# Optimization experiments

Measured on AMD Instinct MI355X. Metric: run time of the kernel, lower is better.

The kernel has to match this reference:

```python
import jax, jax.numpy as jnp
import numpy as np

N_GOOD = 16
NUM_TEST = 16
NUM_UNITS = 32
EPS = 1e-5


def _mlp(x, w1, b1, w2, b2):
    # Linear -> ReLU -> Linear -> ReLU
    h = jax.nn.relu(x @ w1 + b1)
    return jax.nn.relu(h @ w2 + b2)


def _ln_relu(x, g, b):
    mu = jnp.mean(x, axis=-1, keepdims=True)
    var = jnp.mean(jnp.square(x - mu), axis=-1, keepdims=True)
    return jax.nn.relu((x - mu) / jnp.sqrt(var + EPS) * g + b)


def _attend(self_out, enc):
    # self_out: [B, D], enc: [B, N, D]
    scores = jnp.einsum('bd,bnd->bn', self_out, enc) / np.float32(np.sqrt(NUM_TEST))
    attn = jax.nn.softmax(scores, axis=-1)
    return jnp.einsum('bn,bnd->bd', attn, enc)


def setup_inputs() -> dict:
    key = jax.random.key(0)
    ks = jax.random.split(key, 24)
    B = 262144
    obs_dim = 4 + (N_GOOD - 1) * 5 + N_GOOD * 3  # 127

    def lin(k, fan_in, fan_out):
        bound = 1.0 / np.sqrt(fan_in)
        kw, kb = jax.random.split(k)
        w = jax.random.uniform(kw, (fan_in, fan_out), jnp.float32, -bound, bound)
        b = jax.random.uniform(kb, (fan_out,), jnp.float32, -bound, bound)
        return w, b

    en_w1, en_b1 = lin(ks[0], 4, NUM_UNITS)
    en_w2, en_b2 = lin(ks[1], NUM_UNITS, NUM_TEST)
    oa_w1, oa_b1 = lin(ks[2], 5, NUM_UNITS)
    oa_w2, oa_b2 = lin(ks[3], NUM_UNITS, NUM_TEST)
    g_w1, g_b1 = lin(ks[4], 3, NUM_UNITS)
    g_w2, g_b2 = lin(ks[5], NUM_UNITS, NUM_TEST)
    m_w1, m_b1 = lin(ks[6], NUM_TEST * 3, NUM_UNITS)
    m_w2, m_b2 = lin(ks[7], NUM_UNITS, NUM_UNITS)
    m_w3, m_b3 = lin(ks[8], NUM_UNITS, 2)

    return {
        's_input': jax.random.normal(ks[9], (B, obs_dim), jnp.float32),
        'en_w1': en_w1, 'en_b1': en_b1, 'en_w2': en_w2, 'en_b2': en_b2,
        'oa_w1': oa_w1, 'oa_b1': oa_b1, 'oa_w2': oa_w2, 'oa_b2': oa_b2,
        'oa_g': jnp.ones((NUM_TEST,), jnp.float32), 'oa_bln': jnp.zeros((NUM_TEST,), jnp.float32),
        'g_w1': g_w1, 'g_b1': g_b1, 'g_w2': g_w2, 'g_b2': g_b2,
        'g_g': jnp.ones((NUM_TEST,), jnp.float32), 'g_bln': jnp.zeros((NUM_TEST,), jnp.float32),
        'm_w1': m_w1, 'm_b1': m_b1, 'm_w2': m_w2, 'm_b2': m_b2, 'm_w3': m_w3, 'm_b3': m_b3,
    }


def reference(s_input, en_w1, en_b1, en_w2, en_b2,
              oa_w1, oa_b1, oa_w2, oa_b2, oa_g, oa_bln,
              g_w1, g_b1, g_w2, g_b2, g_g, g_bln,
              m_w1, m_b1, m_w2, m_b2, m_w3, m_b3):
    n = N_GOOD
    B = s_input.shape[0]

    # self encoding: [B, 16]
    self_out = _mlp(s_input[:, :4], en_w1, en_b1, en_w2, en_b2)

    # other agents: width (n-1)*5 = [pos pairs | vel pairs | scalar per agent]
    og = s_input[:, 4:4 + (n - 1) * 5]
    pos = og[:, :(n - 1) * 2].reshape(B, n - 1, 2)
    vel = og[:, (n - 1) * 2:(n - 1) * 4].reshape(B, n - 1, 2)
    scal = og[:, (n - 1) * 4:(n - 1) * 5].reshape(B, n - 1, 1)
    other_in = jnp.concatenate([pos, vel, scal], axis=-1)  # [B, n-1, 5]
    other_enc = _mlp(other_in, oa_w1, oa_b1, oa_w2, oa_b2)  # [B, n-1, 16]
    other_out = _ln_relu(_attend(self_out, other_enc), oa_g, oa_bln)

    # food/goals: last n*3 cols, chunks of 3
    food_in = s_input[:, -n * 3:].reshape(B, n, 3)
    food_enc = _mlp(food_in, g_w1, g_b1, g_w2, g_b2)  # [B, n, 16]
    food_out = _ln_relu(_attend(self_out, food_enc), g_g, g_bln)

    merged = jnp.concatenate([self_out, food_out, other_out], axis=1)  # [B, 48]
    h = jax.nn.leaky_relu(merged @ m_w1 + m_b1, 0.01)
    h = jax.nn.leaky_relu(h @ m_w2 + m_b2, 0.01)
    return jnp.tanh(h @ m_w3 + m_b3)  # [B, 2]
```

## Files before the change

### kernel.cpp

```cpp
#include <hip/hip_runtime.h>
#include <math.h>


#define OBS 127
#define XSS 132

typedef _Float16 v4h  __attribute__((ext_vector_type(4)));
typedef __fp16   p2h  __attribute__((ext_vector_type(2)));
typedef float    v16f __attribute__((ext_vector_type(16)));
typedef float    f4u  __attribute__((ext_vector_type(4), aligned(4)));

#define MFMA32(a, b, c) __builtin_amdgcn_mfma_f32_32x32x8f16((a), (b), (c), 0, 0, 0)

union PK { p2h p[2]; v4h h; uint2 u; };
union HU { unsigned u[2]; v4h h; };

__device__ __forceinline__ v4h zero4h() {
    v4h z; z[0] = z[1] = z[2] = z[3] = (_Float16)0.f; return z;
}
__device__ __forceinline__ v4h pack4(float a, float b, float c, float d) {
    PK q;
    q.p[0] = __builtin_amdgcn_cvt_pkrtz(a, b);
    q.p[1] = __builtin_amdgcn_cvt_pkrtz(c, d);
    return q.h;
}
__device__ __forceinline__ v4h a1frag(const float* __restrict__ W,
                                      const float* __restrict__ b,
                                      int kin, int m, int h) {
    v4h r;
    #pragma unroll
    for (int j = 0; j < 4; ++j) {
        const int k = 4 * h + j;
        const float v = (k < kin) ? W[k * 32 + m] : (k == kin ? b[m] : 0.f);
        r[j] = (_Float16)v;
    }
    return r;
}
__device__ __forceinline__ v4h a2frag(const float* __restrict__ W2,
                                      int s, int m, int h) {
    v4h r;
    #pragma unroll
    for (int j = 0; j < 4; ++j) {
        const int k = 8 * s + 4 * h + j;
        r[j] = (_Float16)((m < 16) ? W2[k * 16 + m] : 0.f);
    }
    return r;
}
__device__ __forceinline__ v4h wfrag(const float* __restrict__ W, int ncols,
                                     int K, int s, int m, int h, int colmax) {
    v4h r;
    #pragma unroll
    for (int j = 0; j < 4; ++j) {
        const int k = 8 * s + 4 * h + j;
        r[j] = (_Float16)((k < K && m < colmax) ? W[k * ncols + m] : 0.f);
    }
    return r;
}
__device__ __forceinline__ v4h bfragA(const float* __restrict__ b, int m, int h, int colmax) {
    v4h r = zero4h();
    if (h == 0 && m < colmax) r[0] = (_Float16)b[m];
    return r;
}
__device__ __forceinline__ float fast_tanh(float x) {
    x = fminf(fmaxf(x, -15.f), 15.f);
    const float ex = __expf(2.f * x);
    return (ex - 1.f) / (ex + 1.f);
}

template <int BR>
__device__ __forceinline__ void entity_step(const _Float16* __restrict__ xr,
                                            int e, int h,
                                            v4h A1, const v4h (&A2)[4],
                                            const float (&b2v)[8],
                                            const float (&stl)[8],
                                            float& l, float (&o)[8],
                                            v16f z16) {
    v4h bf = zero4h();
    if (BR == 1) {
        if (h == 0) {
            bf[0] = xr[79 + 3 * e];
            bf[1] = xr[80 + 3 * e];
            bf[2] = xr[81 + 3 * e];
            bf[3] = (_Float16)1.f;
        }
    } else {
        if (h == 0) {
            HU u;
            u.u[0] = *(const unsigned*)(xr + 4 + 2 * e);
            u.u[1] = *(const unsigned*)(xr + 34 + 2 * e);
            bf = u.h;
        } else {
            bf[0] = xr[64 + e];
            bf[1] = (_Float16)1.f;
        }
    }
    const v16f d = MFMA32(A1, bf, z16);
    const v4h p0 = pack4(fmaxf(d[0], 0.f), fmaxf(d[1], 0.f), fmaxf(d[2], 0.f), fmaxf(d[3], 0.f));
    const v4h p1 = pack4(fmaxf(d[4], 0.f), fmaxf(d[5], 0.f), fmaxf(d[6], 0.f), fmaxf(d[7], 0.f));
    const v4h p2 = pack4(fmaxf(d[8], 0.f), fmaxf(d[9], 0.f), fmaxf(d[10], 0.f), fmaxf(d[11], 0.f));
    const v4h p3 = pack4(fmaxf(d[12], 0.f), fmaxf(d[13], 0.f), fmaxf(d[14], 0.f), fmaxf(d[15], 0.f));
    v16f ca = MFMA32(A2[0], p0, z16);
    ca = MFMA32(A2[2], p2, ca);
    v16f cb = MFMA32(A2[1], p1, z16);
    cb = MFMA32(A2[3], p3, cb);
    float e2[8], part = 0.f;
    #pragma unroll
    for (int r = 0; r < 8; ++r) {
        e2[r] = fmaxf(ca[r] + cb[r] + b2v[r], 0.f);
        part += stl[r] * e2[r];
    }
    part += __shfl_xor(part, 32);
    const float p = __builtin_amdgcn_exp2f(part);
    l += p;
    #pragma unroll
    for (int r = 0; r < 8; ++r) o[r] += p * e2[r];
}

__device__ __forceinline__ void ln_fin(float l, const float (&o)[8],
                                       const float (&gv)[8], const float (&blv)[8],
                                       v4h& c0, v4h& c1) {
    const float rl = 1.f / l;
    float a[8], sum = 0.f;
    #pragma unroll
    for (int r = 0; r < 8; ++r) { a[r] = o[r] * rl; sum += a[r]; }
    sum += __shfl_xor(sum, 32);
    const float mu = sum * 0.0625f;
    float var = 0.f;
    #pragma unroll
    for (int r = 0; r < 8; ++r) { a[r] -= mu; var += a[r] * a[r]; }
    var += __shfl_xor(var, 32);
    const float inv = rsqrtf(var * 0.0625f + 1e-5f);
    float v[8];
    #pragma unroll
    for (int r = 0; r < 8; ++r) v[r] = fmaxf(a[r] * inv * gv[r] + blv[r], 0.f);
    c0 = pack4(v[0], v[1], v[2], v[3]);
    c1 = pack4(v[4], v[5], v[6], v[7]);
}

__global__ __launch_bounds__(256)
void actor_mfma(const float* __restrict__ x,
                const float* __restrict__ en_w1, const float* __restrict__ en_b1,
                const float* __restrict__ en_w2, const float* __restrict__ en_b2,
                const float* __restrict__ oa_w1, const float* __restrict__ oa_b1,
                const float* __restrict__ oa_w2, const float* __restrict__ oa_b2,
                const float* __restrict__ oa_g,  const float* __restrict__ oa_bln,
                const float* __restrict__ g_w1,  const float* __restrict__ g_b1,
                const float* __restrict__ g_w2,  const float* __restrict__ g_b2,
                const float* __restrict__ g_g,   const float* __restrict__ g_bln,
                const float* __restrict__ m_w1,  const float* __restrict__ m_b1,
                const float* __restrict__ m_w2,  const float* __restrict__ m_b2,
                const float* __restrict__ m_w3,  const float* __restrict__ m_b3,
                float* __restrict__ out, int B)
{
    const int lane = threadIdx.x & 63, wid = threadIdx.x >> 6;
    const int n = lane & 31, h = lane >> 5;

    __shared__ __align__(16) _Float16 xs_all[4][32 * XSS];
    _Float16* xs = xs_all[wid];

    const int r0 = blockIdx.x * 128 + wid * 32;
    const bool wvalid = (r0 < B);

    if (wvalid) {
        const float* __restrict__ xp = x + (size_t)r0 * OBS;
        if (r0 + 32 <= B) {
            #pragma unroll
            for (int i = 0; i < 16; ++i) {
                const int gI = i * 64 + lane;
                if (gI < 992) {
                    const int row = gI / 31;
                    const int c4 = gI - row * 31;
                    const f4u v = *(const f4u*)(xp + row * 127 + c4 * 4);
                    PK q;
                    q.p[0] = __builtin_amdgcn_cvt_pkrtz(v[0], v[1]);
                    q.p[1] = __builtin_amdgcn_cvt_pkrtz(v[2], v[3]);
                    *(uint2*)(xs + row * XSS + c4 * 4) = q.u;
                }
            }
            #pragma unroll
            for (int t = 0; t < 2; ++t) {
                const int idx = t * 64 + lane;
                if (idx < 96) {
                    const int row = idx / 3;
                    const int c = 124 + idx - row * 3;
                    xs[row * XSS + c] = (_Float16)xp[row * 127 + c];
                }
            }
        } else {
            const int lim = (B - r0) * OBS;
            for (int i = 0; i < 64; ++i) {
                const int f = i * 64 + lane;
                if (f < lim) {
                    const int r = f / 127;
                    xs[f + 5 * r] = (_Float16)xp[f];
                }
            }
        }
    }
    __syncthreads();

    v16f z16;
    #pragma unroll
    for (int r = 0; r < 16; ++r) z16[r] = 0.f;

    const v4h sA1 = a1frag(en_w1, en_b1, 4, n, h);
    v4h sA2[4], fA2[4], oA2[4];
    #pragma unroll
    for (int s = 0; s < 4; ++s) {
        sA2[s] = a2frag(en_w2, s, n, h);
        fA2[s] = a2frag(g_w2, s, n, h);
        oA2[s] = a2frag(oa_w2, s, n, h);
    }
    const v4h fA1 = a1frag(g_w1, g_b1, 3, n, h);
    const v4h oA1 = a1frag(oa_w1, oa_b1, 5, n, h);
    float sb2v[8], fb2v[8], ob2v[8];
    #pragma unroll
    for (int r = 0; r < 8; ++r) {
        const int m = (r & 3) + 8 * (r >> 2) + 4 * h;
        sb2v[r] = en_b2[m];
        fb2v[r] = g_b2[m];
        ob2v[r] = oa_b2[m];
    }

    const _Float16* xr = xs + n * XSS;
    float st[8], stl[8];
    v4h Bs0, Bs1;
    {
        v4h bs = zero4h();
        if (h == 0) bs = *(const v4h*)xr;
        else        bs[0] = (_Float16)1.f;
        const v16f d = MFMA32(sA1, bs, z16);
        const v4h p0 = pack4(fmaxf(d[0], 0.f), fmaxf(d[1], 0.f), fmaxf(d[2], 0.f), fmaxf(d[3], 0.f));
        const v4h p1 = pack4(fmaxf(d[4], 0.f), fmaxf(d[5], 0.f), fmaxf(d[6], 0.f), fmaxf(d[7], 0.f));
        const v4h p2 = pack4(fmaxf(d[8], 0.f), fmaxf(d[9], 0.f), fmaxf(d[10], 0.f), fmaxf(d[11], 0.f));
        const v4h p3 = pack4(fmaxf(d[12], 0.f), fmaxf(d[13], 0.f), fmaxf(d[14], 0.f), fmaxf(d[15], 0.f));
        v16f ca = MFMA32(sA2[0], p0, z16);
        ca = MFMA32(sA2[2], p2, ca);
        v16f cb = MFMA32(sA2[1], p1, z16);
        cb = MFMA32(sA2[3], p3, cb);
        const float SK = 0.25f * 1.44269504088896f;
        #pragma unroll
        for (int r = 0; r < 8; ++r) {
            st[r] = fmaxf(ca[r] + cb[r] + sb2v[r], 0.f);
            stl[r] = st[r] * SK;
        }
        Bs0 = pack4(st[0], st[1], st[2], st[3]);
        Bs1 = pack4(st[4], st[5], st[6], st[7]);
    }

    float lf = 0.f, lo = 0.f;
    float of[8], oo[8];
    #pragma unroll
    for (int r = 0; r < 8; ++r) { of[r] = 0.f; oo[r] = 0.f; }
    #pragma unroll 2
    for (int e = 0; e < 16; ++e) {
        entity_step<1>(xr, e, h, fA1, fA2, fb2v, stl, lf, of, z16);
        if (e < 15)
            entity_step<0>(xr, e, h, oA1, oA2, ob2v, stl, lo, oo, z16);
    }

    float fgv[8], fblv[8], ogv[8], oblv[8];
    #pragma unroll
    for (int r = 0; r < 8; ++r) {
        const int m = (r & 3) + 8 * (r >> 2) + 4 * h;
        fgv[r] = g_g[m];  fblv[r] = g_bln[m];
        ogv[r] = oa_g[m]; oblv[r] = oa_bln[m];
    }
    v4h Bf0, Bf1, Bo0, Bo1;
    ln_fin(lf, of, fgv, fblv, Bf0, Bf1);
    ln_fin(lo, oo, ogv, oblv, Bo0, Bo1);

    v4h one_h0 = zero4h();
    if (h == 0) one_h0[0] = (_Float16)1.f;

    v16f m1 = MFMA32(wfrag(m_w1, 32, 48, 0, n, h, 32), Bs0, z16);
    m1 = MFMA32(wfrag(m_w1, 32, 48, 1, n, h, 32), Bs1, m1);
    m1 = MFMA32(wfrag(m_w1, 32, 48, 2, n, h, 32), Bf0, m1);
    m1 = MFMA32(wfrag(m_w1, 32, 48, 3, n, h, 32), Bf1, m1);
    m1 = MFMA32(wfrag(m_w1, 32, 48, 4, n, h, 32), Bo0, m1);
    m1 = MFMA32(wfrag(m_w1, 32, 48, 5, n, h, 32), Bo1, m1);
    m1 = MFMA32(bfragA(m_b1, n, h, 32), one_h0, m1);
    v4h q[4];
    #pragma unroll
    for (int s = 0; s < 4; ++s) {
        float t0 = m1[4 * s],     t1 = m1[4 * s + 1];
        float t2 = m1[4 * s + 2], t3 = m1[4 * s + 3];
        q[s] = pack4(fmaxf(t0, 0.01f * t0), fmaxf(t1, 0.01f * t1),
                     fmaxf(t2, 0.01f * t2), fmaxf(t3, 0.01f * t3));
    }
    v16f m2 = MFMA32(wfrag(m_w2, 32, 32, 0, n, h, 32), q[0], z16);
    m2 = MFMA32(wfrag(m_w2, 32, 32, 1, n, h, 32), q[1], m2);
    m2 = MFMA32(wfrag(m_w2, 32, 32, 2, n, h, 32), q[2], m2);
    m2 = MFMA32(wfrag(m_w2, 32, 32, 3, n, h, 32), q[3], m2);
    m2 = MFMA32(bfragA(m_b2, n, h, 32), one_h0, m2);
    v4h z[4];
    #pragma unroll
    for (int s = 0; s < 4; ++s) {
        float t0 = m2[4 * s],     t1 = m2[4 * s + 1];
        float t2 = m2[4 * s + 2], t3 = m2[4 * s + 3];
        z[s] = pack4(fmaxf(t0, 0.01f * t0), fmaxf(t1, 0.01f * t1),
                     fmaxf(t2, 0.01f * t2), fmaxf(t3, 0.01f * t3));
    }
    v16f m3 = MFMA32(wfrag(m_w3, 2, 32, 0, n, h, 2), z[0], z16);
    m3 = MFMA32(wfrag(m_w3, 2, 32, 1, n, h, 2), z[1], m3);
    m3 = MFMA32(wfrag(m_w3, 2, 32, 2, n, h, 2), z[2], m3);
    m3 = MFMA32(wfrag(m_w3, 2, 32, 3, n, h, 2), z[3], m3);
    m3 = MFMA32(bfragA(m_b3, n, h, 2), one_h0, m3);

    if (h == 0 && wvalid && r0 + n < B) {
        float2 res;
        res.x = fast_tanh(m3[0]);
        res.y = fast_tanh(m3[1]);
        *(float2*)(out + (size_t)(r0 + n) * 2) = res;
    }
}

extern "C" void kernel_launch(void* const* d_in, const int* in_sizes, int n_in,
                              void* d_out, int out_size, void* d_ws, size_t ws_size,
                              hipStream_t stream) {
    const int B = in_sizes[0] / OBS;
    const float* xin = (const float*)d_in[0];
    const float* en_w1 = (const float*)d_in[1];
    const float* en_b1 = (const float*)d_in[2];
    const float* en_w2 = (const float*)d_in[3];
    const float* en_b2 = (const float*)d_in[4];
    const float* oa_w1 = (const float*)d_in[5];
    const float* oa_b1 = (const float*)d_in[6];
    const float* oa_w2 = (const float*)d_in[7];
    const float* oa_b2 = (const float*)d_in[8];
    const float* oa_g  = (const float*)d_in[9];
    const float* oa_bl = (const float*)d_in[10];
    const float* g_w1  = (const float*)d_in[11];
    const float* g_b1  = (const float*)d_in[12];
    const float* g_w2  = (const float*)d_in[13];
    const float* g_b2  = (const float*)d_in[14];
    const float* g_g   = (const float*)d_in[15];
    const float* g_bl  = (const float*)d_in[16];
    const float* m_w1  = (const float*)d_in[17];
    const float* m_b1  = (const float*)d_in[18];
    const float* m_w2  = (const float*)d_in[19];
    const float* m_b2  = (const float*)d_in[20];
    const float* m_w3  = (const float*)d_in[21];
    const float* m_b3  = (const float*)d_in[22];

    const int rows_per_block = 128;
    const int grid = (B + rows_per_block - 1) / rows_per_block;
    actor_mfma<<<grid, 256, 0, stream>>>(
        xin, en_w1, en_b1, en_w2, en_b2,
        oa_w1, oa_b1, oa_w2, oa_b2, oa_g, oa_bl,
        g_w1, g_b1, g_w2, g_b2, g_g, g_bl,
        m_w1, m_b1, m_w2, m_b2, m_w3, m_b3,
        (float*)d_out, B);
}
```

Measured before the change: 304.4 us.

## Switch to 32x32x16 f16 MFMA with permuted weight fragments

Replaces the 32x32x8 f16 MFMA chain with the gfx950 32x32x16 f16 instruction, which halves the MFMA count per entity step and in the merge MLP. The first-layer weight rows are permuted so the first MFMA's output registers line up directly with the K=16 B-operand layout. Merge-MLP biases are now loaded into the accumulator initial value rather than added through an extra bias MFMA. ReLU and leaky-ReLU are applied in packed fp16 after conversion, which changes rounding slightly and adds some register pressure from the wider fragments.

```diff
diff --git a/kernel.cpp b/kernel.cpp
--- a/kernel.cpp
+++ b/kernel.cpp
@@ -6,59 +6,74 @@
 #define XSS 132
 
 typedef _Float16 v4h  __attribute__((ext_vector_type(4)));
+typedef _Float16 v8h  __attribute__((ext_vector_type(8)));
 typedef __fp16   p2h  __attribute__((ext_vector_type(2)));
 typedef float    v16f __attribute__((ext_vector_type(16)));
 typedef float    f4u  __attribute__((ext_vector_type(4), aligned(4)));
 
-#define MFMA32(a, b, c) __builtin_amdgcn_mfma_f32_32x32x8f16((a), (b), (c), 0, 0, 0)
-
-union PK { p2h p[2]; v4h h; uint2 u; };
-union HU { unsigned u[2]; v4h h; };
-
-__device__ __forceinline__ v4h zero4h() {
-    v4h z; z[0] = z[1] = z[2] = z[3] = (_Float16)0.f; return z;
-}
-__device__ __forceinline__ v4h pack4(float a, float b, float c, float d) {
-    PK q;
-    q.p[0] = __builtin_amdgcn_cvt_pkrtz(a, b);
-    q.p[1] = __builtin_amdgcn_cvt_pkrtz(c, d);
+#define MFMA16(a, b, c) __builtin_amdgcn_mfma_f32_32x32x16_f16((a), (b), (c), 0, 0, 0)
+
+union PK8 { p2h p[4]; v8h h; };
+union HU8 { unsigned u[4]; v8h h; _Float16 e[8]; };
+
+__device__ __forceinline__ v8h zero8h() {
+    v8h z;
+    #pragma unroll
+    for (int j = 0; j < 8; ++j) z[j] = (_Float16)0.f;
+    return z;
+}
+__device__ __forceinline__ v8h pk8(const v16f& d, int b) {
+    PK8 q;
+    q.p[0] = __builtin_amdgcn_cvt_pkrtz(d[b],     d[b + 1]);
+    q.p[1] = __builtin_amdgcn_cvt_pkrtz(d[b + 2], d[b + 3]);
+    q.p[2] = __builtin_amdgcn_cvt_pkrtz(d[b + 4], d[b + 5]);
+    q.p[3] = __builtin_amdgcn_cvt_pkrtz(d[b + 6], d[b + 7]);
     return q.h;
 }
-__device__ __forceinline__ v4h a1frag(const float* __restrict__ W,
-                                      const float* __restrict__ b,
-                                      int kin, int m, int h) {
-    v4h r;
-    #pragma unroll
-    for (int j = 0; j < 4; ++j) {
-        const int k = 4 * h + j;
-        const float v = (k < kin) ? W[k * 32 + m] : (k == kin ? b[m] : 0.f);
+__device__ __forceinline__ v8h pkr8(const v16f& d, int b) {
+    return __builtin_elementwise_max(pk8(d, b), zero8h());
+}
+__device__ __forceinline__ v8h pk8f(const float (&v)[8]) {
+    PK8 q;
+    q.p[0] = __builtin_amdgcn_cvt_pkrtz(v[0], v[1]);
+    q.p[1] = __builtin_amdgcn_cvt_pkrtz(v[2], v[3]);
+    q.p[2] = __builtin_amdgcn_cvt_pkrtz(v[4], v[5]);
+    q.p[3] = __builtin_amdgcn_cvt_pkrtz(v[6], v[7]);
+    return q.h;
+}
+__device__ __forceinline__ v8h lrelu8(v8h t) {
+    const v8h s = t * (_Float16)0.01f;
+    return __builtin_elementwise_max(t, s);
+}
+__device__ __forceinline__ v8h a1fragK16(const float* __restrict__ W,
+                                         const float* __restrict__ b,
+                                         int kin, int m, int h) {
+    const int Lm = (m & ~12) | ((m & 4) << 1) | ((m & 8) >> 1);
+    v8h r;
+    #pragma unroll
+    for (int j = 0; j < 8; ++j) {
+        const int k = 8 * h + j;
+        const float v = (k < kin) ? W[k * 32 + Lm] : (k == kin ? b[Lm] : 0.f);
         r[j] = (_Float16)v;
     }
     return r;
 }
-__device__ __forceinline__ v4h a2frag(const float* __restrict__ W2,
-                                      int s, int m, int h) {
-    v4h r;
-    #pragma unroll
-    for (int j = 0; j < 4; ++j) {
-        const int k = 8 * s + 4 * h + j;
-        r[j] = (_Float16)((m < 16) ? W2[k * 16 + m] : 0.f);
-    }
+__device__ __forceinline__ v8h a2fragK16(const float* __restrict__ W2,
+                                         int s, int m, int h) {
+    v8h r;
+    #pragma unroll
+    for (int j = 0; j < 8; ++j)
+        r[j] = (_Float16)((m < 16) ? W2[(16 * s + 8 * h + j) * 16 + m] : 0.f);
     return r;
 }
-__device__ __forceinline__ v4h wfrag(const float* __restrict__ W, int ncols,
-                                     int K, int s, int m, int h, int colmax) {
-    v4h r;
-    #pragma unroll
-    for (int j = 0; j < 4; ++j) {
-        const int k = 8 * s + 4 * h + j;
-        r[j] = (_Float16)((k < K && m < colmax) ? W[k * ncols + m] : 0.f);
-    }
-    return r;
-}
-__device__ __forceinline__ v4h bfragA(const float* __restrict__ b, int m, int h, int colmax) {
-    v4h r = zero4h();
-    if (h == 0 && m < colmax) r[0] = (_Float16)b[m];
+__device__ __forceinline__ v8h mfragK16(const float* __restrict__ W, int ncols,
+                                        int base, int m, int h, int colmax) {
+    v8h r;
+    #pragma unroll
+    for (int j = 0; j < 8; ++j) {
+        const int ch = base + (j & 3) + 8 * (j >> 2) + 4 * h;
+        r[j] = (_Float16)((m < colmax) ? W[ch * ncols + m] : 0.f);
+    }
     return r;
 }
 __device__ __forceinline__ float fast_tanh(float x) {
@@ -70,43 +85,38 @@
 template <int BR>
 __device__ __forceinline__ void entity_step(const _Float16* __restrict__ xr,
                                             int e, int h,
-                                            v4h A1, const v4h (&A2)[4],
+                                            v8h A1, v8h A2a, v8h A2b,
                                             const float (&b2v)[8],
                                             const float (&stl)[8],
                                             float& l, float (&o)[8],
                                             v16f z16) {
-    v4h bf = zero4h();
-    if (BR == 1) {
-        if (h == 0) {
-            bf[0] = xr[79 + 3 * e];
-            bf[1] = xr[80 + 3 * e];
-            bf[2] = xr[81 + 3 * e];
-            bf[3] = (_Float16)1.f;
-        }
-    } else {
-        if (h == 0) {
-            HU u;
+    v8h bf = zero8h();
+    if (h == 0) {
+        HU8 u;
+        #pragma unroll
+        for (int j = 0; j < 4; ++j) u.u[j] = 0;
+        if (BR == 1) {
+            u.e[0] = xr[79 + 3 * e];
+            u.e[1] = xr[80 + 3 * e];
+            u.e[2] = xr[81 + 3 * e];
+            u.e[3] = (_Float16)1.f;
+        } else {
             u.u[0] = *(const unsigned*)(xr + 4 + 2 * e);
             u.u[1] = *(const unsigned*)(xr + 34 + 2 * e);
-            bf = u.h;
-        } else {
-            bf[0] = xr[64 + e];
-            bf[1] = (_Float16)1.f;
+            u.e[4] = xr[64 + e];
+            u.e[5] = (_Float16)1.f;
         }
-    }
-    const v16f d = MFMA32(A1, bf, z16);
-    const v4h p0 = pack4(fmaxf(d[0], 0.f), fmaxf(d[1], 0.f), fmaxf(d[2], 0.f), fmaxf(d[3], 0.f));
-    const v4h p1 = pack4(fmaxf(d[4], 0.f), fmaxf(d[5], 0.f), fmaxf(d[6], 0.f), fmaxf(d[7], 0.f));
-    const v4h p2 = pack4(fmaxf(d[8], 0.f), fmaxf(d[9], 0.f), fmaxf(d[10], 0.f), fmaxf(d[11], 0.f));
-    const v4h p3 = pack4(fmaxf(d[12], 0.f), fmaxf(d[13], 0.f), fmaxf(d[14], 0.f), fmaxf(d[15], 0.f));
-    v16f ca = MFMA32(A2[0], p0, z16);
-    ca = MFMA32(A2[2], p2, ca);
-    v16f cb = MFMA32(A2[1], p1, z16);
-    cb = MFMA32(A2[3], p3, cb);
+        bf = u.h;
+    }
+    const v16f dH = MFMA16(A1, bf, z16);
+    const v8h p0 = pkr8(dH, 0);
+    const v8h p1 = pkr8(dH, 8);
+    v16f c = MFMA16(A2a, p0, z16);
+    c = MFMA16(A2b, p1, c);
     float e2[8], part = 0.f;
     #pragma unroll
     for (int r = 0; r < 8; ++r) {
-        e2[r] = fmaxf(ca[r] + cb[r] + b2v[r], 0.f);
+        e2[r] = fmaxf(c[r] + b2v[r], 0.f);
         part += stl[r] * e2[r];
     }
     part += __shfl_xor(part, 32);
@@ -116,9 +126,8 @@
     for (int r = 0; r < 8; ++r) o[r] += p * e2[r];
 }
 
-__device__ __forceinline__ void ln_fin(float l, const float (&o)[8],
-                                       const float (&gv)[8], const float (&blv)[8],
-                                       v4h& c0, v4h& c1) {
+__device__ __forceinline__ v8h ln_fin(float l, const float (&o)[8],
+                                      const float (&gv)[8], const float (&blv)[8]) {
     const float rl = 1.f / l;
     float a[8], sum = 0.f;
     #pragma unroll
@@ -133,8 +142,7 @@
     float v[8];
     #pragma unroll
     for (int r = 0; r < 8; ++r) v[r] = fmaxf(a[r] * inv * gv[r] + blv[r], 0.f);
-    c0 = pack4(v[0], v[1], v[2], v[3]);
-    c1 = pack4(v[4], v[5], v[6], v[7]);
+    return pk8f(v);
 }
 
 __global__ __launch_bounds__(256)
@@ -171,10 +179,10 @@
                     const int row = gI / 31;
                     const int c4 = gI - row * 31;
                     const f4u v = *(const f4u*)(xp + row * 127 + c4 * 4);
-                    PK q;
+                    PK8 q;
                     q.p[0] = __builtin_amdgcn_cvt_pkrtz(v[0], v[1]);
                     q.p[1] = __builtin_amdgcn_cvt_pkrtz(v[2], v[3]);
-                    *(uint2*)(xs + row * XSS + c4 * 4) = q.u;
+                    *(uint2*)(xs + row * XSS + c4 * 4) = *(const uint2*)&q;
                 }
             }
             #pragma unroll
@@ -203,16 +211,6 @@
     #pragma unroll
     for (int r = 0; r < 16; ++r) z16[r] = 0.f;
 
-    const v4h sA1 = a1frag(en_w1, en_b1, 4, n, h);
-    v4h sA2[4], fA2[4], oA2[4];
-    #pragma unroll
-    for (int s = 0; s < 4; ++s) {
-        sA2[s] = a2frag(en_w2, s, n, h);
-        fA2[s] = a2frag(g_w2, s, n, h);
-        oA2[s] = a2frag(oa_w2, s, n, h);
-    }
-    const v4h fA1 = a1frag(g_w1, g_b1, 3, n, h);
-    const v4h oA1 = a1frag(oa_w1, oa_b1, 5, n, h);
     float sb2v[8], fb2v[8], ob2v[8];
     #pragma unroll
     for (int r = 0; r < 8; ++r) {
@@ -224,39 +222,49 @@
 
     const _Float16* xr = xs + n * XSS;
     float st[8], stl[8];
-    v4h Bs0, Bs1;
+    v8h Bs;
     {
-        v4h bs = zero4h();
-        if (h == 0) bs = *(const v4h*)xr;
-        else        bs[0] = (_Float16)1.f;
-        const v16f d = MFMA32(sA1, bs, z16);
-        const v4h p0 = pack4(fmaxf(d[0], 0.f), fmaxf(d[1], 0.f), fmaxf(d[2], 0.f), fmaxf(d[3], 0.f));
-        const v4h p1 = pack4(fmaxf(d[4], 0.f), fmaxf(d[5], 0.f), fmaxf(d[6], 0.f), fmaxf(d[7], 0.f));
-        const v4h p2 = pack4(fmaxf(d[8], 0.f), fmaxf(d[9], 0.f), fmaxf(d[10], 0.f), fmaxf(d[11], 0.f));
-        const v4h p3 = pack4(fmaxf(d[12], 0.f), fmaxf(d[13], 0.f), fmaxf(d[14], 0.f), fmaxf(d[15], 0.f));
-        v16f ca = MFMA32(sA2[0], p0, z16);
-        ca = MFMA32(sA2[2], p2, ca);
-        v16f cb = MFMA32(sA2[1], p1, z16);
-        cb = MFMA32(sA2[3], p3, cb);
+        const v8h sA1 = a1fragK16(en_w1, en_b1, 4, n, h);
+        const v8h sA2a = a2fragK16(en_w2, 0, n, h);
+        const v8h sA2b = a2fragK16(en_w2, 1, n, h);
+        v8h bs = zero8h();
+        if (h == 0) {
+            HU8 u;
+            #pragma unroll
+            for (int j = 0; j < 4; ++j) u.u[j] = 0;
+            *(uint2*)&u.u[0] = *(const uint2*)xr;
+            u.e[4] = (_Float16)1.f;
+            bs = u.h;
+        }
+        const v16f dS = MFMA16(sA1, bs, z16);
+        v16f cS = MFMA16(sA2a, pkr8(dS, 0), z16);
+        cS = MFMA16(sA2b, pkr8(dS, 8), cS);
         const float SK = 0.25f * 1.44269504088896f;
+        float sv[8];
         #pragma unroll
         for (int r = 0; r < 8; ++r) {
-            st[r] = fmaxf(ca[r] + cb[r] + sb2v[r], 0.f);
-            stl[r] = st[r] * SK;
+            sv[r] = fmaxf(cS[r] + sb2v[r], 0.f);
+            st[r] = sv[r];
+            stl[r] = sv[r] * SK;
         }
-        Bs0 = pack4(st[0], st[1], st[2], st[3]);
-        Bs1 = pack4(st[4], st[5], st[6], st[7]);
-    }
-
-    float lf = 0.f, lo = 0.f;
-    float of[8], oo[8];
+        Bs = pk8f(sv);
+    }
+
+    const v8h fA1 = a1fragK16(g_w1, g_b1, 3, n, h);
+    const v8h fA2a = a2fragK16(g_w2, 0, n, h);
+    const v8h fA2b = a2fragK16(g_w2, 1, n, h);
+    const v8h oA1 = a1fragK16(oa_w1, oa_b1, 5, n, h);
+    const v8h oA2a = a2fragK16(oa_w2, 0, n, h);
+    const v8h oA2b = a2fragK16(oa_w2, 1, n, h);
+
+    float lf = 0.f, lo = 0.f, of[8], oo[8];
     #pragma unroll
     for (int r = 0; r < 8; ++r) { of[r] = 0.f; oo[r] = 0.f; }
     #pragma unroll 2
     for (int e = 0; e < 16; ++e) {
-        entity_step<1>(xr, e, h, fA1, fA2, fb2v, stl, lf, of, z16);
+        entity_step<1>(xr, e, h, fA1, fA2a, fA2b, fb2v, stl, lf, of, z16);
         if (e < 15)
-            entity_step<0>(xr, e, h, oA1, oA2, ob2v, stl, lo, oo, z16);
+            entity_step<0>(xr, e, h, oA1, oA2a, oA2b, ob2v, stl, lo, oo, z16);
     }
 
     float fgv[8], fblv[8], ogv[8], oblv[8];
@@ -266,51 +274,32 @@
         fgv[r] = g_g[m];  fblv[r] = g_bln[m];
         ogv[r] = oa_g[m]; oblv[r] = oa_bln[m];
     }
-    v4h Bf0, Bf1, Bo0, Bo1;
-    ln_fin(lf, of, fgv, fblv, Bf0, Bf1);
-    ln_fin(lo, oo, ogv, oblv, Bo0, Bo1);
-
-    v4h one_h0 = zero4h();
-    if (h == 0) one_h0[0] = (_Float16)1.f;
-
-    v16f m1 = MFMA32(wfrag(m_w1, 32, 48, 0, n, h, 32), Bs0, z16);
-    m1 = MFMA32(wfrag(m_w1, 32, 48, 1, n, h, 32), Bs1, m1);
-    m1 = MFMA32(wfrag(m_w1, 32, 48, 2, n, h, 32), Bf0, m1);
-    m1 = MFMA32(wfrag(m_w1, 32, 48, 3, n, h, 32), Bf1, m1);
-    m1 = MFMA32(wfrag(m_w1, 32, 48, 4, n, h, 32), Bo0, m1);
-    m1 = MFMA32(wfrag(m_w1, 32, 48, 5, n, h, 32), Bo1, m1);
-    m1 = MFMA32(bfragA(m_b1, n, h, 32), one_h0, m1);
-    v4h q[4];
-    #pragma unroll
-    for (int s = 0; s < 4; ++s) {
-        float t0 = m1[4 * s],     t1 = m1[4 * s + 1];
-        float t2 = m1[4 * s + 2], t3 = m1[4 * s + 3];
-        q[s] = pack4(fmaxf(t0, 0.01f * t0), fmaxf(t1, 0.01f * t1),
-                     fmaxf(t2, 0.01f * t2), fmaxf(t3, 0.01f * t3));
-    }
-    v16f m2 = MFMA32(wfrag(m_w2, 32, 32, 0, n, h, 32), q[0], z16);
-    m2 = MFMA32(wfrag(m_w2, 32, 32, 1, n, h, 32), q[1], m2);
-    m2 = MFMA32(wfrag(m_w2, 32, 32, 2, n, h, 32), q[2], m2);
-    m2 = MFMA32(wfrag(m_w2, 32, 32, 3, n, h, 32), q[3], m2);
-    m2 = MFMA32(bfragA(m_b2, n, h, 32), one_h0, m2);
-    v4h z[4];
-    #pragma unroll
-    for (int s = 0; s < 4; ++s) {
-        float t0 = m2[4 * s],     t1 = m2[4 * s + 1];
-        float t2 = m2[4 * s + 2], t3 = m2[4 * s + 3];
-        z[s] = pack4(fmaxf(t0, 0.01f * t0), fmaxf(t1, 0.01f * t1),
-                     fmaxf(t2, 0.01f * t2), fmaxf(t3, 0.01f * t3));
-    }
-    v16f m3 = MFMA32(wfrag(m_w3, 2, 32, 0, n, h, 2), z[0], z16);
-    m3 = MFMA32(wfrag(m_w3, 2, 32, 1, n, h, 2), z[1], m3);
-    m3 = MFMA32(wfrag(m_w3, 2, 32, 2, n, h, 2), z[2], m3);
-    m3 = MFMA32(wfrag(m_w3, 2, 32, 3, n, h, 2), z[3], m3);
-    m3 = MFMA32(bfragA(m_b3, n, h, 2), one_h0, m3);
+    const v8h Bf = ln_fin(lf, of, fgv, fblv);
+    const v8h Bo = ln_fin(lo, oo, ogv, oblv);
+
+    v16f m1C, m2C;
+    #pragma unroll
+    for (int r = 0; r < 16; ++r) {
+        const int m = (r & 3) + 8 * (r >> 2) + 4 * h;
+        m1C[r] = m_b1[m];
+        m2C[r] = m_b2[m];
+    }
+    v16f m1 = MFMA16(mfragK16(m_w1, 32, 0, n, h, 32), Bs, m1C);
+    m1 = MFMA16(mfragK16(m_w1, 32, 16, n, h, 32), Bf, m1);
+    m1 = MFMA16(mfragK16(m_w1, 32, 32, n, h, 32), Bo, m1);
+    const v8h q0 = lrelu8(pk8(m1, 0));
+    const v8h q1 = lrelu8(pk8(m1, 8));
+    v16f m2 = MFMA16(mfragK16(m_w2, 32, 0, n, h, 32), q0, m2C);
+    m2 = MFMA16(mfragK16(m_w2, 32, 16, n, h, 32), q1, m2);
+    const v8h z0 = lrelu8(pk8(m2, 0));
+    const v8h z1 = lrelu8(pk8(m2, 8));
+    v16f m3 = MFMA16(mfragK16(m_w3, 2, 0, n, h, 2), z0, z16);
+    m3 = MFMA16(mfragK16(m_w3, 2, 16, n, h, 2), z1, m3);
 
     if (h == 0 && wvalid && r0 + n < B) {
         float2 res;
-        res.x = fast_tanh(m3[0]);
-        res.y = fast_tanh(m3[1]);
+        res.x = fast_tanh(m3[0] + m_b3[0]);
+        res.y = fast_tanh(m3[1] + m_b3[1]);
         *(float2*)(out + (size_t)(r0 + n) * 2) = res;
     }
 }
```

New measurement: 298.0 us. 1.02x faster.
